# Optimization experiments

Measured on AMD Instinct MI355X. Metric: run time of the kernel, lower is better.

## Reference

```python
import jax, jax.numpy as jnp
import numpy as np

B, L, D, V, d, N, H = 16, 1024, 50, 129, 64, 2, 8
DK = d // H           # 8
DFF = 2 * d           # 128
CVE = int(np.sqrt(d)) # 8
EPS = 1e-07 ** 2      # module squares epsilon
MASK_ATTN = -1e-30    # Transformer mask_value (as in source)
MASK_POOL = -1e+30    # Attention-pooling mask_value


def setup_inputs() -> dict:
    key = jax.random.key(0)
    ks = jax.random.split(key, 32)
    g = lambda i, shape, s=0.02: (jax.random.normal(ks[i], shape, dtype=jnp.float32) * s)
    inp = {
        'demo':   jax.random.normal(ks[0], (B, D), dtype=jnp.float32),
        'times':  jax.random.uniform(ks[1], (B, L), dtype=jnp.float32),
        'values': jax.random.normal(ks[2], (B, L), dtype=jnp.float32),
        'varis':  jax.random.randint(ks[3], (B, L), 0, V + 1),
        # variable embedding table
        'emb': g(4, (V + 1, d), 0.05),
        # CVE for values: Linear(1,CVE)+tanh+Linear(CVE,d,no bias)
        'vW1': g(5, (1, CVE), 0.5), 'vb1': jnp.zeros((CVE,), jnp.float32), 'vW2': g(6, (CVE, d), 0.1),
        # CVE for times
        'tW1': g(7, (1, CVE), 0.5), 'tb1': jnp.zeros((CVE,), jnp.float32), 'tW2': g(8, (CVE, d), 0.1),
        # Transformer params
        'Wq': g(9,  (N, H, d, DK), 0.1), 'Wk': g(10, (N, H, d, DK), 0.1),
        'Wv': g(11, (N, H, d, DK), 0.1), 'Wo': g(12, (N, H * DK, d), 0.1),
        'W1': g(13, (N, d, DFF), 0.1), 'b1': jnp.zeros((N, DFF), jnp.float32),
        'W2': g(14, (N, DFF, d), 0.1), 'b2': jnp.zeros((N, d), jnp.float32),
        'gamma': jnp.ones((2 * N,), jnp.float32), 'beta': jnp.zeros((2 * N,), jnp.float32),
        # Attention pooling: Linear(d,2d)+tanh+Linear(2d,1,no bias)
        'aW1': g(15, (d, 2 * d), 0.1), 'ab1': jnp.zeros((2 * d,), jnp.float32), 'aW2': g(16, (2 * d, 1), 0.1),
        # demo stack: Linear(D,2d)+tanh+Linear(2d,d)+tanh
        'dW1': g(17, (D, 2 * d), 0.1), 'db1': jnp.zeros((2 * d,), jnp.float32),
        'dW2': g(18, (2 * d, d), 0.1), 'db2': jnp.zeros((d,), jnp.float32),
        # output head: Linear(2d,1)+sigmoid+flatten
        'Wout': g(19, (2 * d, 1), 0.1), 'bout': jnp.zeros((1,), jnp.float32),
    }
    return inp


def _ln(X, g, b):
    mean = jnp.mean(X, axis=-1, keepdims=True)
    var = jnp.mean(jnp.square(X - mean), axis=-1, keepdims=True)
    return (X - mean) / jnp.sqrt(var + EPS) * g + b


def _forward(demo, times, values, varis, emb, vW1, vb1, vW2, tW1, tb1, tW2,
             Wq, Wk, Wv, Wo, W1, b1, W2, b2, gamma, beta,
             aW1, ab1, aW2, dW1, db1, dW2, db2, Wout, bout):
    mask = (varis > 0).astype(jnp.float32)  # [B,L]
    demo_enc = jnp.tanh(jnp.tanh(demo @ dW1 + db1) @ dW2 + db2)  # [B,d]
    varis_emb = emb[varis]                                       # [B,L,d]
    values_emb = jnp.tanh(values[..., None] @ vW1 + vb1) @ vW2   # [B,L,d]
    times_emb = jnp.tanh(times[..., None] @ tW1 + tb1) @ tW2     # [B,L,d]
    X = varis_emb + values_emb + times_emb

    mb = mask[:, None, None, :]  # [B,1,1,L] broadcasts over heads & query rows
    for i in range(N):
        q = jnp.einsum('bld,hdk->bhlk', X, Wq[i])
        k = jnp.einsum('bld,hdk->bhlk', X, Wk[i])
        v = jnp.einsum('bld,hdk->bhlk', X, Wv[i])
        A = jnp.einsum('bhlk,bhmk->bhlm', q, k)      # no 1/sqrt(dk) scaling (faithful)
        A = mb * A + (1.0 - mb) * MASK_ATTN
        A = jax.nn.softmax(A, axis=-1)
        O = jnp.einsum('bhlm,bhmk->bhlk', A, v)      # [B,H,L,DK]
        conc = jnp.transpose(O, (0, 2, 1, 3)).reshape(O.shape[0], O.shape[2], H * DK)
        X = X + conc @ Wo[i]
        X = _ln(X, gamma[2 * i], beta[2 * i])
        ffn = jax.nn.relu(X @ W1[i] + b1[i]) @ W2[i] + b2[i]
        X = X + ffn
        X = _ln(X, gamma[2 * i + 1], beta[2 * i + 1])

    aw = jnp.tanh(X @ aW1 + ab1) @ aW2               # [B,L,1]
    m = mask[..., None]
    aw = jax.nn.softmax(m * aw + (1.0 - m) * MASK_POOL, axis=-2)
    fused = jnp.sum(X * aw, axis=-2)                 # [B,d]
    conc = jnp.concatenate([fused, demo_enc], axis=-1)
    return jax.nn.sigmoid(conc @ Wout + bout).reshape(-1)  # [B]


def reference(demo, times, values, varis, emb, vW1, vb1, vW2, tW1, tb1, tW2,
              Wq, Wk, Wv, Wo, W1, b1, W2, b2, gamma, beta,
              aW1, ab1, aW2, dW1, db1, dW2, db2, Wout, bout):
    return _forward(demo, times, values, varis, emb, vW1, vb1, vW2, tW1, tb1, tW2,
                    Wq, Wk, Wv, Wo, W1, b1, W2, b2, gamma, beta,
                    aW1, ab1, aW2, dW1, db1, dW2, db2, Wout, bout)
```

## Files before the change

### kernel.cpp

```cpp
#include <hip/hip_runtime.h>
#include <math.h>


typedef __bf16 bf16x8 __attribute__((ext_vector_type(8)));
typedef __bf16 bf16x2 __attribute__((ext_vector_type(2)));
typedef float f32x16 __attribute__((ext_vector_type(16)));
typedef unsigned int uint4e __attribute__((ext_vector_type(4)));
typedef unsigned long long u64;

static __device__ __forceinline__ float wave_sum64(float x) {
#pragma unroll
    for (int off = 32; off > 0; off >>= 1) x += __shfl_xor(x, off, 64);
    return x;
}

static __device__ __forceinline__ unsigned pack2(float a, float b) {
    bf16x2 t; t[0] = (__bf16)a; t[1] = (__bf16)b;
    return __builtin_bit_cast(unsigned, t);
}

static __device__ __forceinline__ float b2f(__bf16 h) {
    unsigned short us = __builtin_bit_cast(unsigned short, h);
    unsigned u = ((unsigned)us) << 16;
    return __builtin_bit_cast(float, u);
}

static __device__ __forceinline__ float exp2fast(float x) {
#if defined(__has_builtin) && __has_builtin(__builtin_amdgcn_exp2f)
    return __builtin_amdgcn_exp2f(x);
#else
    return exp2f(x);
#endif
}

static __device__ __forceinline__ void plswap(unsigned v, unsigned& lo, unsigned& hi_) {
#if defined(__has_builtin) && __has_builtin(__builtin_amdgcn_permlane32_swap)
    auto r = __builtin_amdgcn_permlane32_swap(v, v, false, false);
    lo = r[0]; hi_ = r[1];
#else
    unsigned x = __shfl_xor(v, 32, 64);
    bool h = (threadIdx.x & 32) != 0;
    lo = h ? x : v;
    hi_ = h ? v : x;
#endif
}

__global__ __launch_bounds__(256) void embed_demo_kernel(
    const float* __restrict__ times, const float* __restrict__ values,
    const int* __restrict__ varis, const float* __restrict__ emb,
    const float* __restrict__ vW1, const float* __restrict__ vb1, const float* __restrict__ vW2,
    const float* __restrict__ tW1, const float* __restrict__ tb1, const float* __restrict__ tW2,
    const float* __restrict__ demo, const float* __restrict__ dW1, const float* __restrict__ db1,
    const float* __restrict__ dW2, const float* __restrict__ db2,
    float* __restrict__ X, float* __restrict__ mask, float* __restrict__ denc)
{
    __shared__ float sh[128];
    int tid = threadIdx.x;
    if (blockIdx.x < 4096) {
        int row = blockIdx.x * 4 + (tid >> 6);
        int c   = tid & 63;
        float v = values[row];
        float t = times[row];
        int var = varis[row];
        if (c == 0) mask[row] = (var > 0) ? 1.0f : 0.0f;
        float th = 0.f;
        if (c < 8)       th = tanhf(fmaf(v, vW1[c], vb1[c]));
        else if (c < 16) th = tanhf(fmaf(t, tW1[c - 8], tb1[c - 8]));
        float acc = emb[var * 64 + c];
#pragma unroll
        for (int j = 0; j < 8; ++j) {
            acc = fmaf(__shfl(th, j, 64),     vW2[j * 64 + c], acc);
            acc = fmaf(__shfl(th, j + 8, 64), tW2[j * 64 + c], acc);
        }
        X[row * 64 + c] = acc;
    } else {
        int b = blockIdx.x - 4096;
        if (tid < 128) {
            float a = db1[tid];
            for (int j = 0; j < 50; ++j) a = fmaf(demo[b * 50 + j], dW1[j * 128 + tid], a);
            sh[tid] = tanhf(a);
        }
        __syncthreads();
        if (tid < 64) {
            float a2 = db2[tid];
#pragma unroll 8
            for (int j = 0; j < 128; ++j) a2 = fmaf(sh[j], dW2[j * 64 + tid], a2);
            denc[b * 64 + tid] = tanhf(a2);
        }
    }
}

__global__ __launch_bounds__(256) void qkv_kernel(
    const float* __restrict__ X, const float* __restrict__ mask,
    const float* __restrict__ Wq, const float* __restrict__ Wk, const float* __restrict__ Wv,
    __bf16* __restrict__ qbf, __bf16* __restrict__ kbf, __bf16* __restrict__ vtb)
{
    __shared__ __align__(16) unsigned char qsm[52224];
    float* sWq = (float*)qsm;
    float* sWk = sWq + 4352;
    float* sWv = sWk + 4352;
    int tid = threadIdx.x;
    for (int idx = tid; idx < 4096; idx += 256) {
        int h = idx >> 9, c = (idx >> 3) & 63, kk = idx & 7;
        int o = h * 8 + kk;
        sWq[o * 68 + c] = Wq[idx];
        sWk[o * 68 + c] = Wk[idx];
        sWv[o * 68 + c] = Wv[idx];
    }
    int row0 = blockIdx.x * 16;
    __syncthreads();
    int lane = tid & 63;
    int wv4 = (tid >> 6) * 4;
    float aq[4] = {0.f, 0.f, 0.f, 0.f};
    float ak[4] = {0.f, 0.f, 0.f, 0.f};
    float av[4] = {0.f, 0.f, 0.f, 0.f};
#pragma unroll
    for (int c = 0; c < 64; c += 4) {
        float4 xv[4];
#pragma unroll
        for (int rr = 0; rr < 4; ++rr)
            xv[rr] = *(const float4*)(X + (row0 + wv4 + rr) * 64 + c);
        float4 wq = *(const float4*)(sWq + lane * 68 + c);
        float4 wk = *(const float4*)(sWk + lane * 68 + c);
        float4 wvv= *(const float4*)(sWv + lane * 68 + c);
#pragma unroll
        for (int rr = 0; rr < 4; ++rr) {
            aq[rr] = fmaf(xv[rr].x, wq.x, aq[rr]);  aq[rr] = fmaf(xv[rr].y, wq.y, aq[rr]);
            aq[rr] = fmaf(xv[rr].z, wq.z, aq[rr]);  aq[rr] = fmaf(xv[rr].w, wq.w, aq[rr]);
            ak[rr] = fmaf(xv[rr].x, wk.x, ak[rr]);  ak[rr] = fmaf(xv[rr].y, wk.y, ak[rr]);
            ak[rr] = fmaf(xv[rr].z, wk.z, ak[rr]);  ak[rr] = fmaf(xv[rr].w, wk.w, ak[rr]);
            av[rr] = fmaf(xv[rr].x, wvv.x, av[rr]); av[rr] = fmaf(xv[rr].y, wvv.y, av[rr]);
            av[rr] = fmaf(xv[rr].z, wvv.z, av[rr]); av[rr] = fmaf(xv[rr].w, wvv.w, av[rr]);
        }
    }
    float aqr[4], akr[4], avr[4];
#pragma unroll
    for (int rr = 0; rr < 4; ++rr) {
        float km = mask[row0 + wv4 + rr];
        aqr[rr] = aq[rr] * 1.4426950408889634f;
        akr[rr] = (km != 0.f) ? ak[rr] : 0.f;
        avr[rr] = av[rr];
    }
    __syncthreads();
    __bf16* sQb = (__bf16*)qsm;
    __bf16* sKb = (__bf16*)(qsm + 2304);
    __bf16* sVt = (__bf16*)(qsm + 4608);
    int h = lane >> 3, kk = lane & 7;
#pragma unroll
    for (int rr = 0; rr < 4; ++rr) {
        int r = wv4 + rr;
        sQb[h * 136 + r * 8 + kk] = (__bf16)aqr[rr];
        sKb[h * 136 + r * 8 + kk] = (__bf16)akr[rr];
        sVt[lane * 18 + r] = (__bf16)avr[rr];
    }
    __syncthreads();
    int b = row0 >> 10, l0 = row0 & 1023;
    unsigned* qg = (unsigned*)qbf;
    unsigned* kg = (unsigned*)kbf;
    const unsigned* q32 = (const unsigned*)sQb;
    const unsigned* k32 = (const unsigned*)sKb;
#pragma unroll
    for (int it = 0; it < 2; ++it) {
        int idx = it * 256 + tid;
        int hh = idx >> 6, w = idx & 63;
        int gbase = ((b * 8 + hh) * 1024 + l0) * 4;
        qg[gbase + w] = q32[hh * 68 + w];
        kg[gbase + w] = k32[hh * 68 + w];
    }
#pragma unroll
    for (int it = 0; it < 2; ++it) {
        int idx = it * 256 + tid;
        int hkk = idx >> 3, lp = idx & 7;
        unsigned w = ((const unsigned*)sVt)[hkk * 9 + lp];
        int hh = hkk >> 3, k2 = hkk & 7;
        ((unsigned*)(vtb + (b * 8 + hh) * 8192 + k2 * 1024 + l0))[lp] = w;
    }
}

__global__ __launch_bounds__(256, 2) void attn_mfma_kernel(
    const __bf16* __restrict__ qbf, const __bf16* __restrict__ kbf,
    const __bf16* __restrict__ vtb, float* __restrict__ O)
{
    __shared__ __align__(16) unsigned char smem[35008];
    __bf16* sK  = (__bf16*)smem;
    __bf16* sVT = (__bf16*)(smem + 16384);

    int tid   = threadIdx.x;
    int bh    = blockIdx.x & 127;
    int chunk = blockIdx.x >> 7;

    const u64* kg = (const u64*)(kbf + bh * 8192);
    u64* sKq = (u64*)sK;
#pragma unroll
    for (int i = 0; i < 8; ++i) sKq[i * 256 + tid] = kg[i * 256 + tid];

    const u64* vgb = (const u64*)(vtb + bh * 8192);
#pragma unroll
    for (int it = 0; it < 8; ++it) {
        int idx = it * 256 + tid;
        int r = idx >> 8, w = idx & 255;
        ((u64*)(sVT + r * 1032))[w] = vgb[idx];
    }
    {
        unsigned* p1 = (unsigned*)(sVT + 8 * 1032);
        p1[tid] = 0x3f803f80u;
        p1[256 + tid] = 0x3f803f80u;
    }
    __syncthreads();

    int lane = tid & 63;
    int wv   = tid >> 6;
    int hi   = lane >> 5;
    int l31  = lane & 31;
    unsigned hm = hi ? 0u : 0xffffffffu;

    int qrow = chunk * 128 + wv * 32 + l31;

    bf16x8 qf;
    {
        const __bf16* qp = qbf + (bh * 1024 + qrow) * 8;
        uint4e qa = *(const uint4e*)qp;
        qa[0] &= hm; qa[1] &= hm; qa[2] &= hm; qa[3] &= hm;
        qf = __builtin_bit_cast(bf16x8, qa);
    }

    f32x16 acc, zc;
#pragma unroll
    for (int i = 0; i < 16; ++i) { acc[i] = 0.f; zc[i] = 0.f; }

    const bf16x8* sKv = (const bf16x8*)sK;
    const __bf16* vbase = sVT + (l31 < 8 ? l31 : 8) * 1032;

    bf16x8 kf = sKv[l31];
#pragma unroll 2
    for (int kt = 0; kt < 32; ++kt) {
        bf16x8 kfn = sKv[((kt + 1) & 31) * 32 + l31];
        f32x16 st = __builtin_amdgcn_mfma_f32_32x32x16_bf16(kf, qf, zc, 0, 0, 0);
        float p[16];
#pragma unroll
        for (int r = 0; r < 16; ++r) p[r] = exp2fast(st[r]);

#pragma unroll
        for (int h = 0; h < 2; ++h) {
            unsigned La0, Ha0, Lb0, Hb0, La1, Ha1, Lb1, Hb1;
            int g0 = 2 * h, g1 = 2 * h + 1;
            plswap(pack2(p[4 * g0 + 0], p[4 * g0 + 1]), La0, Ha0);
            plswap(pack2(p[4 * g0 + 2], p[4 * g0 + 3]), Lb0, Hb0);
            plswap(pack2(p[4 * g1 + 0], p[4 * g1 + 1]), La1, Ha1);
            plswap(pack2(p[4 * g1 + 2], p[4 * g1 + 3]), Lb1, Hb1);
            uint4e pw;
            pw[0] = hi ? La1 : La0;
            pw[1] = hi ? Lb1 : Lb0;
            pw[2] = hi ? Ha1 : Ha0;
            pw[3] = hi ? Hb1 : Hb0;
            bf16x8 vf = *(const bf16x8*)(vbase + kt * 32 + 16 * h + 8 * hi);
            acc = __builtin_amdgcn_mfma_f32_32x32x16_bf16(vf, __builtin_bit_cast(bf16x8, pw), acc, 0, 0, 0);
        }
        kf = kfn;
    }

    float inv = 1.0f / acc[4];
    __syncthreads();
    float* sO = (float*)smem;
    int qloc = wv * 32 + l31;
    float4 t0;
    t0.x = acc[0] * inv; t0.y = acc[1] * inv; t0.z = acc[2] * inv; t0.w = acc[3] * inv;
    *(float4*)(sO + qloc * 12 + 4 * hi) = t0;
    __syncthreads();
    float* og = O + (bh * 1024 + chunk * 128) * 8;
    {
        int q = tid >> 1, part = tid & 1;
        *(float4*)(og + tid * 4) = *(const float4*)(sO + q * 12 + part * 4);
    }
}

__global__ __launch_bounds__(512) void tail_kernel(
    float* __restrict__ X, const float* __restrict__ O, const float* __restrict__ Wo,
    const float* __restrict__ W1, const float* __restrict__ b1,
    const float* __restrict__ W2, const float* __restrict__ b2,
    const float* __restrict__ gamma, const float* __restrict__ beta, int gi,
    const float* __restrict__ aW1, const float* __restrict__ ab1,
    const float* __restrict__ aW2, float* __restrict__ aw, int doAw)
{
    __shared__ __align__(16) float sW[128 * 68];
    __shared__ __align__(16) float sX[2048];
    __shared__ __align__(16) unsigned char sHraw[8704];
    int tid = threadIdx.x;
    int row0 = blockIdx.x * 32;
    int lane = tid & 63, wave = tid >> 6;
    float* sHo = (float*)sHraw;
    __bf16* sHb = (__bf16*)sHraw;
    float* sHout = (float*)sHraw;

    for (int idx = tid; idx < 4096; idx += 512) {
        int j = idx >> 6, c = idx & 63;
        sW[c * 68 + j] = Wo[idx];
    }
#pragma unroll
    for (int it = 0; it < 4; ++it) {
        int idx = it * 512 + tid;
        int r = idx >> 6, j = idx & 63;
        int grow = row0 + r;
        int b = grow >> 10, l = grow & 1023;
        int bh = b * 8 + (j >> 3);
        sHo[r * 68 + j] = O[(bh * 1024 + l) * 8 + (j & 7)];
    }
    ((float4*)sX)[tid] = ((const float4*)(X + row0 * 64))[tid];
    __syncthreads();

    {
        int c4 = tid & 15, r = tid >> 4;
        float acc[4] = {0.f, 0.f, 0.f, 0.f};
#pragma unroll 2
        for (int j = 0; j < 64; j += 4) {
            float4 hv = *(const float4*)(sHo + r * 68 + j);
#pragma unroll
            for (int cc = 0; cc < 4; ++cc) {
                float4 wv = *(const float4*)(sW + (c4 + 16 * cc) * 68 + j);
                acc[cc] = fmaf(hv.x, wv.x, acc[cc]); acc[cc] = fmaf(hv.y, wv.y, acc[cc]);
                acc[cc] = fmaf(hv.z, wv.z, acc[cc]); acc[cc] = fmaf(hv.w, wv.w, acc[cc]);
            }
        }
#pragma unroll
        for (int cc = 0; cc < 4; ++cc)
            sX[r * 64 + c4 + 16 * cc] += acc[cc];
    }
    __syncthreads();
#pragma unroll
    for (int it = 0; it < 4; ++it) {
        int r = wave * 4 + it;
        float x = sX[r * 64 + lane];
        float mean = wave_sum64(x) * (1.0f / 64.0f);
        float dx = x - mean;
        float var = wave_sum64(dx * dx) * (1.0f / 64.0f);
        sX[r * 64 + lane] = dx * rsqrtf(var + 1e-14f) * gamma[gi] + beta[gi];
    }
    __syncthreads();

    for (int idx = tid; idx < 8192; idx += 512) {
        int c = idx >> 7, j = idx & 127;
        sW[j * 68 + c] = W1[idx];
    }
    __syncthreads();
    {
        int j4 = tid & 31;
        int r0 = (tid >> 5) * 2;
        float acc[2][4];
#pragma unroll
        for (int jj = 0; jj < 4; ++jj) {
            float bb = b1[j4 + 32 * jj];
            acc[0][jj] = bb; acc[1][jj] = bb;
        }
#pragma unroll 2
        for (int c = 0; c < 64; c += 4) {
            float4 xv0 = *(const float4*)(sX + r0 * 64 + c);
            float4 xv1 = *(const float4*)(sX + (r0 + 1) * 64 + c);
#pragma unroll
            for (int jj = 0; jj < 4; ++jj) {
                float4 wv = *(const float4*)(sW + (j4 + 32 * jj) * 68 + c);
                acc[0][jj] = fmaf(xv0.x, wv.x, acc[0][jj]); acc[0][jj] = fmaf(xv0.y, wv.y, acc[0][jj]);
                acc[0][jj] = fmaf(xv0.z, wv.z, acc[0][jj]); acc[0][jj] = fmaf(xv0.w, wv.w, acc[0][jj]);
                acc[1][jj] = fmaf(xv1.x, wv.x, acc[1][jj]); acc[1][jj] = fmaf(xv1.y, wv.y, acc[1][jj]);
                acc[1][jj] = fmaf(xv1.z, wv.z, acc[1][jj]); acc[1][jj] = fmaf(xv1.w, wv.w, acc[1][jj]);
            }
        }
#pragma unroll
        for (int rr = 0; rr < 2; ++rr)
#pragma unroll
            for (int jj = 0; jj < 4; ++jj)
                sHb[(r0 + rr) * 136 + j4 + 32 * jj] = (__bf16)fmaxf(acc[rr][jj], 0.0f);
    }
    __syncthreads();
    for (int idx = tid; idx < 8192; idx += 512) {
        int j = idx >> 6, c = idx & 63;
        sW[c * 132 + j] = W2[idx];
    }
    __syncthreads();
    int c4 = tid & 15;
    int rrow = tid >> 4;
    float acc2[4];
#pragma unroll
    for (int cc = 0; cc < 4; ++cc) acc2[cc] = b2[c4 + 16 * cc];
#pragma unroll 2
    for (int jc = 0; jc < 128; jc += 8) {
        float hf[8];
        bf16x8 hb = *(const bf16x8*)(sHb + rrow * 136 + jc);
#pragma unroll
        for (int e = 0; e < 8; ++e) hf[e] = b2f(hb[e]);
#pragma unroll
        for (int cc = 0; cc < 4; ++cc) {
            float4 w0 = *(const float4*)(sW + (c4 + 16 * cc) * 132 + jc);
            float4 w1 = *(const float4*)(sW + (c4 + 16 * cc) * 132 + jc + 4);
            acc2[cc] = fmaf(hf[0], w0.x, acc2[cc]); acc2[cc] = fmaf(hf[1], w0.y, acc2[cc]);
            acc2[cc] = fmaf(hf[2], w0.z, acc2[cc]); acc2[cc] = fmaf(hf[3], w0.w, acc2[cc]);
            acc2[cc] = fmaf(hf[4], w1.x, acc2[cc]); acc2[cc] = fmaf(hf[5], w1.y, acc2[cc]);
            acc2[cc] = fmaf(hf[6], w1.z, acc2[cc]); acc2[cc] = fmaf(hf[7], w1.w, acc2[cc]);
        }
    }
    __syncthreads();
#pragma unroll
    for (int cc = 0; cc < 4; ++cc)
        sHout[rrow * 64 + c4 + 16 * cc] = acc2[cc];
    __syncthreads();
#pragma unroll
    for (int it = 0; it < 4; ++it) {
        int r = wave * 4 + it;
        float x = sX[r * 64 + lane] + sHout[r * 64 + lane];
        float mean = wave_sum64(x) * (1.0f / 64.0f);
        float dx = x - mean;
        float var = wave_sum64(dx * dx) * (1.0f / 64.0f);
        float xo = dx * rsqrtf(var + 1e-14f) * gamma[gi + 1] + beta[gi + 1];
        X[(row0 + r) * 64 + lane] = xo;
        if (doAw) sX[r * 64 + lane] = xo;
    }
    if (!doAw) return;

    __syncthreads();
    for (int idx = tid; idx < 8192; idx += 512) {
        int c = idx >> 7, j = idx & 127;
        sW[j * 68 + c] = aW1[idx];
    }
    __syncthreads();
    {
        int j4 = tid & 31;
        int r0 = (tid >> 5) * 2;
        float acc[2][4];
#pragma unroll
        for (int jj = 0; jj < 4; ++jj) {
            float bb = ab1[j4 + 32 * jj];
            acc[0][jj] = bb; acc[1][jj] = bb;
        }
#pragma unroll 2
        for (int c = 0; c < 64; c += 4) {
            float4 xv0 = *(const float4*)(sX + r0 * 64 + c);
            float4 xv1 = *(const float4*)(sX + (r0 + 1) * 64 + c);
#pragma unroll
            for (int jj = 0; jj < 4; ++jj) {
                float4 wv = *(const float4*)(sW + (j4 + 32 * jj) * 68 + c);
                acc[0][jj] = fmaf(xv0.x, wv.x, acc[0][jj]); acc[0][jj] = fmaf(xv0.y, wv.y, acc[0][jj]);
                acc[0][jj] = fmaf(xv0.z, wv.z, acc[0][jj]); acc[0][jj] = fmaf(xv0.w, wv.w, acc[0][jj]);
                acc[1][jj] = fmaf(xv1.x, wv.x, acc[1][jj]); acc[1][jj] = fmaf(xv1.y, wv.y, acc[1][jj]);
                acc[1][jj] = fmaf(xv1.z, wv.z, acc[1][jj]); acc[1][jj] = fmaf(xv1.w, wv.w, acc[1][jj]);
            }
        }
        float a2[4];
#pragma unroll
        for (int jj = 0; jj < 4; ++jj) a2[jj] = aW2[j4 + 32 * jj];
#pragma unroll
        for (int rr = 0; rr < 2; ++rr) {
            float part = tanhf(acc[rr][0]) * a2[0] + tanhf(acc[rr][1]) * a2[1]
                       + tanhf(acc[rr][2]) * a2[2] + tanhf(acc[rr][3]) * a2[3];
#pragma unroll
            for (int off = 16; off > 0; off >>= 1) part += __shfl_xor(part, off, 64);
            if ((lane & 31) == 0) aw[row0 + r0 + rr] = part;
        }
    }
}

__global__ __launch_bounds__(1024) void pool_kernel(
    const float* __restrict__ X, const float* __restrict__ aw, const float* __restrict__ mask,
    const float* __restrict__ denc, const float* __restrict__ Wout,
    const float* __restrict__ bout, float* __restrict__ out)
{
    __shared__ float sp[1024];
    __shared__ float red[16];
    __shared__ float red2[16];
    __shared__ float sf[16][64];
    int b = blockIdx.x, tid = threadIdx.x;
    float s = (mask[b * 1024 + tid] != 0.0f) ? aw[b * 1024 + tid] : -1e30f;
    float m = s;
#pragma unroll
    for (int off = 32; off > 0; off >>= 1) m = fmaxf(m, __shfl_xor(m, off, 64));
    if ((tid & 63) == 0) red[tid >> 6] = m;
    __syncthreads();
    float gmax = red[0];
#pragma unroll
    for (int i = 1; i < 16; ++i) gmax = fmaxf(gmax, red[i]);
    float p = __expf(s - gmax);
    sp[tid] = p;
    float psum = wave_sum64(p);
    if ((tid & 63) == 0) red2[tid >> 6] = psum;
    __syncthreads();
    float tot = 0.f;
#pragma unroll
    for (int i = 0; i < 16; ++i) tot += red2[i];
    float inv = 1.0f / tot;
    int c = tid & 63, g = tid >> 6;
    int l0 = g * 64;
    float f = 0.f;
#pragma unroll 4
    for (int i = 0; i < 64; ++i)
        f = fmaf(sp[l0 + i], X[(b * 1024 + l0 + i) * 64 + c], f);
    sf[g][c] = f;
    __syncthreads();
    if (tid < 64) {
        float fc = 0.f;
#pragma unroll
        for (int ch = 0; ch < 16; ++ch) fc += sf[ch][tid];
        fc *= inv;
        float contrib = fc * Wout[tid] + denc[b * 64 + tid] * Wout[64 + tid];
        contrib = wave_sum64(contrib);
        if (tid == 0) out[b] = 1.0f / (1.0f + __expf(-(contrib + bout[0])));
    }
}

extern "C" void kernel_launch(void* const* d_in, const int* in_sizes, int n_in,
                              void* d_out, int out_size, void* d_ws, size_t ws_size,
                              hipStream_t stream)
{
    const float* demo  = (const float*)d_in[0];
    const float* times = (const float*)d_in[1];
    const float* values= (const float*)d_in[2];
    const int*   varis = (const int*)d_in[3];
    const float* emb   = (const float*)d_in[4];
    const float* vW1   = (const float*)d_in[5];
    const float* vb1   = (const float*)d_in[6];
    const float* vW2   = (const float*)d_in[7];
    const float* tW1   = (const float*)d_in[8];
    const float* tb1   = (const float*)d_in[9];
    const float* tW2   = (const float*)d_in[10];
    const float* Wq    = (const float*)d_in[11];
    const float* Wk    = (const float*)d_in[12];
    const float* Wv    = (const float*)d_in[13];
    const float* Wo    = (const float*)d_in[14];
    const float* W1    = (const float*)d_in[15];
    const float* b1    = (const float*)d_in[16];
    const float* W2    = (const float*)d_in[17];
    const float* b2    = (const float*)d_in[18];
    const float* gamma = (const float*)d_in[19];
    const float* beta  = (const float*)d_in[20];
    const float* aW1   = (const float*)d_in[21];
    const float* ab1   = (const float*)d_in[22];
    const float* aW2   = (const float*)d_in[23];
    const float* dW1   = (const float*)d_in[24];
    const float* db1   = (const float*)d_in[25];
    const float* dW2   = (const float*)d_in[26];
    const float* db2   = (const float*)d_in[27];
    const float* Wout  = (const float*)d_in[28];
    const float* bout  = (const float*)d_in[29];
    float* out = (float*)d_out;

    float* ws     = (float*)d_ws;
    float* X      = ws;
    float* mask   = X + 1048576;
    __bf16* qbf   = (__bf16*)(mask + 16384);
    __bf16* kbf   = qbf + 1048576;
    __bf16* vtb   = kbf + 1048576;
    float* Ob     = (float*)(vtb + 1048576);
    float* awb    = Ob + 1048576;
    float* denc   = awb + 16384;

    embed_demo_kernel<<<4112, 256, 0, stream>>>(times, values, varis, emb, vW1, vb1, vW2,
                                                tW1, tb1, tW2, demo, dW1, db1, dW2, db2,
                                                X, mask, denc);
    for (int i = 0; i < 2; ++i) {
        qkv_kernel<<<1024, 256, 0, stream>>>(X, mask, Wq + i * 4096, Wk + i * 4096, Wv + i * 4096,
                                             qbf, kbf, vtb);
        attn_mfma_kernel<<<1024, 256, 0, stream>>>(qbf, kbf, vtb, Ob);
        tail_kernel<<<512, 512, 0, stream>>>(X, Ob, Wo + i * 4096,
                                             W1 + i * 8192, b1 + i * 128, W2 + i * 8192, b2 + i * 64,
                                             gamma, beta, 2 * i,
                                             aW1, ab1, aW2, awb, (i == 1) ? 1 : 0);
    }
    pool_kernel<<<16, 1024, 0, stream>>>(X, awb, mask, denc, Wout, bout, out);
}
```

Measured before the change: 160.4 us.

## Prefetch next-stage weights into registers to overlap global loads with compute

Each weight matrix (W1, W2, aW1) is now loaded from global memory into 16 registers per thread one stage early, so the load runs while the previous matmul executes. The values are then written into the shared weight buffer after the barrier, which removes one __syncthreads per stage. The cost is higher register pressure (48 extra floats live across stages), which could lower occupancy or cause spills in a 512-thread block.

```diff
diff --git a/kernel.cpp b/kernel.cpp
--- a/kernel.cpp
+++ b/kernel.cpp
@@ -306,6 +306,9 @@
         sHo[r * 68 + j] = O[(bh * 1024 + l) * 8 + (j & 7)];
     }
     ((float4*)sX)[tid] = ((const float4*)(X + row0 * 64))[tid];
+    float w1r[16];
+#pragma unroll
+    for (int it = 0; it < 16; ++it) w1r[it] = W1[it * 512 + tid];
     __syncthreads();
 
     {
@@ -326,6 +329,12 @@
             sX[r * 64 + c4 + 16 * cc] += acc[cc];
     }
     __syncthreads();
+#pragma unroll
+    for (int it = 0; it < 16; ++it) {
+        int idx = it * 512 + tid;
+        int c = idx >> 7, j = idx & 127;
+        sW[j * 68 + c] = w1r[it];
+    }
 #pragma unroll
     for (int it = 0; it < 4; ++it) {
         int r = wave * 4 + it;
@@ -335,13 +344,11 @@
         float var = wave_sum64(dx * dx) * (1.0f / 64.0f);
         sX[r * 64 + lane] = dx * rsqrtf(var + 1e-14f) * gamma[gi] + beta[gi];
     }
-    __syncthreads();
-
-    for (int idx = tid; idx < 8192; idx += 512) {
-        int c = idx >> 7, j = idx & 127;
-        sW[j * 68 + c] = W1[idx];
-    }
-    __syncthreads();
+    float w2r[16];
+#pragma unroll
+    for (int it = 0; it < 16; ++it) w2r[it] = W2[it * 512 + tid];
+    __syncthreads();
+
     {
         int j4 = tid & 31;
         int r0 = (tid >> 5) * 2;
@@ -371,11 +378,19 @@
                 sHb[(r0 + rr) * 136 + j4 + 32 * jj] = (__bf16)fmaxf(acc[rr][jj], 0.0f);
     }
     __syncthreads();
-    for (int idx = tid; idx < 8192; idx += 512) {
+#pragma unroll
+    for (int it = 0; it < 16; ++it) {
+        int idx = it * 512 + tid;
         int j = idx >> 6, c = idx & 63;
-        sW[c * 132 + j] = W2[idx];
-    }
-    __syncthreads();
+        sW[c * 132 + j] = w2r[it];
+    }
+    float a1r[16];
+    if (doAw) {
+#pragma unroll
+        for (int it = 0; it < 16; ++it) a1r[it] = aW1[it * 512 + tid];
+    }
+    __syncthreads();
+
     int c4 = tid & 15;
     int rrow = tid >> 4;
     float acc2[4];
@@ -416,9 +431,11 @@
     if (!doAw) return;
 
     __syncthreads();
-    for (int idx = tid; idx < 8192; idx += 512) {
+#pragma unroll
+    for (int it = 0; it < 16; ++it) {
+        int idx = it * 512 + tid;
         int c = idx >> 7, j = idx & 127;
-        sW[j * 68 + c] = aW1[idx];
+        sW[j * 68 + c] = a1r[it];
     }
     __syncthreads();
     {
```

Result: no change. 158.4 us (-1.3%).
